# Optimization experiments

Measured on AMD Instinct MI355X. Metric: run time of the kernel, lower is better.

## Reference

```python
import jax, jax.numpy as jnp
import numpy as np

HEADS = 8
DIM_HEAD = 64


def setup_inputs() -> dict:
    key = jax.random.key(0)
    ks = jax.random.split(key, 6)
    B, Nq, Nk, Dq = 4, 2048, 2048, 1024
    inner = HEADS * DIM_HEAD  # 512
    return {
        "x": jax.random.normal(ks[0], (B, Nq, Dq), jnp.float32),
        "context": jax.random.normal(ks[1], (B, Nk, Dq), jnp.float32),
        "Wq": jax.random.normal(ks[2], (Dq, inner), jnp.float32) * 0.02,
        "Wkv": jax.random.normal(ks[3], (Dq, 2 * inner), jnp.float32) * 0.02,
        "Wout": jax.random.normal(ks[4], (inner, Dq), jnp.float32) * 0.02,
        "bout": jax.random.normal(ks[5], (Dq,), jnp.float32) * 0.02,
        "topk": 64,
    }


def reference(x, context, Wq, Wkv, Wout, bout, topk):
    B, Nq, _ = x.shape
    Nk = context.shape[1]
    H, D = HEADS, DIM_HEAD
    scale = D ** -0.5

    # projections: b n (h d) -> b h n d
    q = (x @ Wq).reshape(B, Nq, H, D).transpose(0, 2, 1, 3)
    kv = context @ Wkv
    k, v = jnp.split(kv, 2, axis=-1)
    k = k.reshape(B, Nk, H, D).transpose(0, 2, 1, 3)
    v = v.reshape(B, Nk, H, D).transpose(0, 2, 1, 3)

    sim = jnp.einsum('bhid,bhjd->bhij', q, k) * scale  # [B,H,Nq,Nk]

    # top-k sparsification: keep only topk keys per query, mask rest to -max
    k_eff = min(int(topk), Nk)
    _, idx = jax.lax.top_k(sim, k_eff)  # [B,H,Nq,k_eff]
    keep = jnp.zeros(sim.shape, dtype=bool)
    bi = jnp.arange(B)[:, None, None, None]
    hi = jnp.arange(H)[None, :, None, None]
    qi = jnp.arange(Nq)[None, None, :, None]
    keep = keep.at[bi, hi, qi, idx].set(True)
    max_neg = -jnp.finfo(sim.dtype).max
    sim = jnp.where(keep, sim, max_neg)

    attn = jax.nn.softmax(sim, axis=-1)
    out = jnp.einsum('bhij,bhjd->bhid', attn, v)
    out = out.transpose(0, 2, 1, 3).reshape(B, Nq, H * D)
    return out @ Wout + bout
```

## Files before the change

kernel.cpp:

```cpp
#include <hip/hip_runtime.h>
#include <math.h>

#define BATCH 4
#define NQ 2048
#define NK 2048
#define DQ 1024
#define NHEADS 8
#define DHEAD 64
#define INNER (NHEADS*DHEAD)
#define NROWS (BATCH*NHEADS*NQ)
#define CAND_MAX 128

using frag_ab = __attribute__((ext_vector_type(8))) short;
using frag_cd = __attribute__((ext_vector_type(4))) float;
using u16x8   = __attribute__((ext_vector_type(8))) unsigned short;

static __device__ __forceinline__ unsigned short f32_to_bf16_rne(float f) {
  unsigned u = __float_as_uint(f);
  u += 0x7FFFu + ((u >> 16) & 1u);
  return (unsigned short)(u >> 16);
}

static __device__ __forceinline__ void split_trunc(float f, unsigned short& h, unsigned short& l) {
  unsigned u = __float_as_uint(f);
  h = (unsigned short)(u >> 16);
  float hf = __uint_as_float(u & 0xFFFF0000u);
  unsigned r = __float_as_uint(f - hf);
  l = (unsigned short)(r >> 16);
}

static __device__ __forceinline__ void split3(float f, unsigned short& h,
                                              unsigned short& m, unsigned short& l) {
  unsigned u = __float_as_uint(f);
  h = (unsigned short)(u >> 16);
  float hf = __uint_as_float(u & 0xFFFF0000u);
  float r1 = f - hf;
  unsigned u1 = __float_as_uint(r1);
  m = (unsigned short)(u1 >> 16);
  float mf = __uint_as_float(u1 & 0xFFFF0000u);
  float r2 = r1 - mf;
  l = (unsigned short)(__float_as_uint(r2) >> 16);
}

__global__ __launch_bounds__(256) void split_wT3(
    const float* __restrict__ W, int ldw, int coloff, int K, int N,
    unsigned short* __restrict__ TH, unsigned short* __restrict__ TM,
    unsigned short* __restrict__ TL)
{
  __shared__ float tile[32*33];
  const int k0 = blockIdx.x * 32, n0 = blockIdx.y * 32;
  const int t = threadIdx.x;
  {
    int lk = t >> 3, ln4 = (t & 7) * 4;
    const float4 v = *(const float4*)(W + (size_t)(k0 + lk)*ldw + coloff + n0 + ln4);
    tile[lk*33 + ln4+0] = v.x;
    tile[lk*33 + ln4+1] = v.y;
    tile[lk*33 + ln4+2] = v.z;
    tile[lk*33 + ln4+3] = v.w;
  }
  __syncthreads();
  int n = t >> 3, k4 = (t & 7) * 4;
  #pragma unroll
  for (int j = 0; j < 4; ++j) {
    unsigned short h, m, l;
    split3(tile[(k4+j)*33 + n], h, m, l);
    size_t o = (size_t)(n0 + n)*K + k0 + k4 + j;
    TH[o] = h; TM[o] = m; TL[o] = l;
  }
}

__global__ __launch_bounds__(256) void split_wT(
    const float* __restrict__ W, int ldw, int coloff, int K, int N,
    unsigned short* __restrict__ TH, unsigned short* __restrict__ TL)
{
  __shared__ float tile[32*33];
  const int k0 = blockIdx.x * 32, n0 = blockIdx.y * 32;
  const int t = threadIdx.x;
  {
    int lk = t >> 3, ln4 = (t & 7) * 4;
    const float4 v = *(const float4*)(W + (size_t)(k0 + lk)*ldw + coloff + n0 + ln4);
    tile[lk*33 + ln4+0] = v.x;
    tile[lk*33 + ln4+1] = v.y;
    tile[lk*33 + ln4+2] = v.z;
    tile[lk*33 + ln4+3] = v.w;
  }
  __syncthreads();
  int n = t >> 3, k4 = (t & 7) * 4;
  #pragma unroll
  for (int j = 0; j < 4; ++j) {
    unsigned short h, l;
    split_trunc(tile[(k4+j)*33 + n], h, l);
    TH[(size_t)(n0 + n)*K + k0 + k4 + j] = h;
    TL[(size_t)(n0 + n)*K + k0 + k4 + j] = l;
  }
}

__global__ __launch_bounds__(512) void gemm_mfma6_proj(
    const float* __restrict__ A0,
    const unsigned short* __restrict__ BtH0, const unsigned short* __restrict__ BtM0,
    const unsigned short* __restrict__ BtL0,
    float* __restrict__ C0_, unsigned short* __restrict__ Hi0, unsigned short* __restrict__ Lo0,
    const float* __restrict__ A1,
    const unsigned short* __restrict__ BtH1, const unsigned short* __restrict__ BtM1,
    const unsigned short* __restrict__ BtL1,
    float* __restrict__ C1_, unsigned short* __restrict__ Hi1, unsigned short* __restrict__ Lo1)
{
  extern __shared__ unsigned short smp[];
  unsigned short* ah = smp;
  unsigned short* am = ah + 128*40;
  unsigned short* al = am + 128*40;
  unsigned short* bh = al + 128*40;
  unsigned short* bm = bh + 128*40;
  unsigned short* bl = bm + 128*40;

  const int t = threadIdx.x;
  const int w = t >> 6, l = t & 63;
  const int lr = l & 15, quad = l >> 4;
  const int bid = (int)blockIdx.x;
  const int half = bid >> 8;
  const int b2 = bid & 255;
  const int lid = (b2 & 7) * 32 + (b2 >> 3);
  const int n0 = (lid & 3) * 128, m0 = (lid >> 2) * 128;

  const float* A = half ? A1 : A0;
  const unsigned short* BtH = half ? BtH1 : BtH0;
  const unsigned short* BtM = half ? BtM1 : BtM0;
  const unsigned short* BtL = half ? BtL1 : BtL0;
  float* C32 = half ? C1_ : C0_;
  unsigned short* Hi = half ? Hi1 : Hi0;
  unsigned short* Lo = half ? Lo1 : Lo0;

  frag_cd acc[8];
  #pragma unroll
  for (int nt = 0; nt < 8; ++nt)
    acc[nt] = (frag_cd){0.f, 0.f, 0.f, 0.f};

  for (int kt = 0; kt < DQ; kt += 32) {
    {
      int row = t >> 2, k8 = (t & 3) * 8;
      const float* src = A + (size_t)(m0 + row) * DQ + kt + k8;
      float4 v0 = *(const float4*)(src);
      float4 v1 = *(const float4*)(src + 4);
      float vv[8] = {v0.x, v0.y, v0.z, v0.w, v1.x, v1.y, v1.z, v1.w};
      unsigned short h8[8], m8[8], l8[8];
      #pragma unroll
      for (int j = 0; j < 8; ++j) split3(vv[j], h8[j], m8[j], l8[j]);
      *(u16x8*)(ah + row*40 + k8) = *(u16x8*)h8;
      *(u16x8*)(am + row*40 + k8) = *(u16x8*)m8;
      *(u16x8*)(al + row*40 + k8) = *(u16x8*)l8;
    }
    {
      int n = t >> 2, k8 = (t & 3) * 8;
      size_t o = (size_t)(n0 + n)*DQ + kt + k8;
      *(u16x8*)(bh + n*40 + k8) = *(const u16x8*)(BtH + o);
      *(u16x8*)(bm + n*40 + k8) = *(const u16x8*)(BtM + o);
      *(u16x8*)(bl + n*40 + k8) = *(const u16x8*)(BtL + o);
    }
    __syncthreads();
    {
      int row = w*16 + lr;
      frag_ab aH = *(const frag_ab*)(ah + row*40 + quad*8);
      frag_ab aM = *(const frag_ab*)(am + row*40 + quad*8);
      frag_ab aL = *(const frag_ab*)(al + row*40 + quad*8);
      #pragma unroll
      for (int nt = 0; nt < 8; ++nt) {
        int bn = nt*16 + lr;
        frag_ab bH_ = *(const frag_ab*)(bh + bn*40 + quad*8);
        frag_ab bM_ = *(const frag_ab*)(bm + bn*40 + quad*8);
        frag_ab bL_ = *(const frag_ab*)(bl + bn*40 + quad*8);
        frag_cd c = acc[nt];
        c = __builtin_amdgcn_mfma_f32_16x16x32_bf16(aL, bH_, c, 0, 0, 0);
        c = __builtin_amdgcn_mfma_f32_16x16x32_bf16(aH, bL_, c, 0, 0, 0);
        c = __builtin_amdgcn_mfma_f32_16x16x32_bf16(aM, bM_, c, 0, 0, 0);
        c = __builtin_amdgcn_mfma_f32_16x16x32_bf16(aM, bH_, c, 0, 0, 0);
        c = __builtin_amdgcn_mfma_f32_16x16x32_bf16(aH, bM_, c, 0, 0, 0);
        c = __builtin_amdgcn_mfma_f32_16x16x32_bf16(aH, bH_, c, 0, 0, 0);
        acc[nt] = c;
      }
    }
    __syncthreads();
  }

  #pragma unroll
  for (int nt = 0; nt < 8; ++nt) {
    int cc = n0 + nt*16 + lr;
    int h = cc >> 6, d = cc & 63;
    #pragma unroll
    for (int i = 0; i < 4; ++i) {
      int r = m0 + w*16 + quad*4 + i;
      int b = r >> 11, n = r & (NQ - 1);
      size_t idx = (((size_t)(b*NHEADS + h))*NQ + n)*64 + d;
      float vf = acc[nt][i];
      C32[idx] = vf;
      unsigned short hb = f32_to_bf16_rne(vf);
      float hf = __uint_as_float((unsigned)hb << 16);
      unsigned short lb = f32_to_bf16_rne(vf - hf);
      Hi[idx] = hb;
      Lo[idx] = lb;
    }
  }
}

template<int MODE>
__global__ __launch_bounds__(512) void gemm_mfma3(
    const float* __restrict__ A, int lda,
    const unsigned short* __restrict__ BtH, const unsigned short* __restrict__ BtL,
    int K, int N, const float* __restrict__ bias, float* __restrict__ C0)
{
  __shared__ unsigned short ah[128*40];
  __shared__ unsigned short al[128*40];
  __shared__ unsigned short bh2[128*40];
  __shared__ unsigned short bl2[128*40];
  const int t = threadIdx.x;
  const int w = t >> 6, l = t & 63;
  const int lr = l & 15, quad = l >> 4;
  const int nx = N >> 7;
  const int bid = (int)blockIdx.x;
  const int nwg = (int)gridDim.x;
  const int lid = (bid & 7) * (nwg >> 3) + (bid >> 3);
  const int n0 = (lid % nx) * 128, m0 = (lid / nx) * 128;

  frag_cd acc[8];
  #pragma unroll
  for (int nt = 0; nt < 8; ++nt)
    acc[nt] = (frag_cd){0.f, 0.f, 0.f, 0.f};

  for (int kt = 0; kt < K; kt += 32) {
    {
      int row = t >> 2, k8 = (t & 3) * 8;
      const float* src = A + (size_t)(m0 + row) * lda + kt + k8;
      float4 v0 = *(const float4*)(src);
      float4 v1 = *(const float4*)(src + 4);
      float vv[8] = {v0.x, v0.y, v0.z, v0.w, v1.x, v1.y, v1.z, v1.w};
      unsigned short h8[8], l8[8];
      #pragma unroll
      for (int j = 0; j < 8; ++j) split_trunc(vv[j], h8[j], l8[j]);
      *(u16x8*)(ah + row*40 + k8) = *(u16x8*)h8;
      *(u16x8*)(al + row*40 + k8) = *(u16x8*)l8;
    }
    {
      int n = t >> 2, k8 = (t & 3) * 8;
      size_t o = (size_t)(n0 + n)*K + kt + k8;
      *(u16x8*)(bh2 + n*40 + k8) = *(const u16x8*)(BtH + o);
      *(u16x8*)(bl2 + n*40 + k8) = *(const u16x8*)(BtL + o);
    }
    __syncthreads();
    {
      int row = w*16 + lr;
      frag_ab aH = *(const frag_ab*)(ah + row*40 + quad*8);
      frag_ab aL = *(const frag_ab*)(al + row*40 + quad*8);
      #pragma unroll
      for (int nt = 0; nt < 8; ++nt) {
        int bn = nt*16 + lr;
        frag_ab bH_ = *(const frag_ab*)(bh2 + bn*40 + quad*8);
        frag_ab bL_ = *(const frag_ab*)(bl2 + bn*40 + quad*8);
        acc[nt] = __builtin_amdgcn_mfma_f32_16x16x32_bf16(aH, bH_, acc[nt], 0, 0, 0);
        acc[nt] = __builtin_amdgcn_mfma_f32_16x16x32_bf16(aH, bL_, acc[nt], 0, 0, 0);
        acc[nt] = __builtin_amdgcn_mfma_f32_16x16x32_bf16(aL, bH_, acc[nt], 0, 0, 0);
      }
    }
    __syncthreads();
  }

  #pragma unroll
  for (int nt = 0; nt < 8; ++nt) {
    int cc = n0 + nt*16 + lr;
    #pragma unroll
    for (int i = 0; i < 4; ++i) {
      int r = m0 + w*16 + quad*4 + i;
      float v = acc[nt][i];
      if (MODE == 0) {
        C0[(size_t)r * N + cc] = v + bias[cc];
      } else {
        int b = r >> 11, n = r & (NQ - 1);
        int h = cc >> 6, d = cc & 63;
        C0[(((size_t)(b*NHEADS + h))*NK + n)*64 + d] = v;
      }
    }
  }
}

__global__ __launch_bounds__(512) void score_mfma(
    const unsigned short* __restrict__ Qhi, const unsigned short* __restrict__ Qlo,
    const unsigned short* __restrict__ Khi, const unsigned short* __restrict__ Klo,
    unsigned short* __restrict__ S16, int bh0)
{
  extern __shared__ unsigned short sm[];
  unsigned short* qh = sm;
  unsigned short* ql = qh + 128*72;
  unsigned short* kh = ql + 128*72;
  unsigned short* kl = kh + 128*72;

  const int t  = threadIdx.x;
  const int qt = blockIdx.x, kt = blockIdx.y;
  const int bh = bh0 + blockIdx.z;
  const size_t qbase = ((size_t)bh*NQ + qt*128) * 64;
  const size_t kbase = ((size_t)bh*NK + kt*128) * 64;

  #pragma unroll
  for (int i = 0; i < 2; ++i) {
    int c   = t + i*512;
    int row = c >> 3, off = (c & 7) * 8;
    *(u16x8*)(qh + row*72 + off) = *(const u16x8*)(Qhi + qbase + row*64 + off);
    *(u16x8*)(ql + row*72 + off) = *(const u16x8*)(Qlo + qbase + row*64 + off);
    *(u16x8*)(kh + row*72 + off) = *(const u16x8*)(Khi + kbase + row*64 + off);
    *(u16x8*)(kl + row*72 + off) = *(const u16x8*)(Klo + kbase + row*64 + off);
  }
  __syncthreads();

  const int w = t >> 6, l = t & 63;
  const int quad = l >> 4, lr = l & 15;

  frag_ab aH[2], aL[2];
  {
    int row = w*16 + lr;
    #pragma unroll
    for (int s = 0; s < 2; ++s) {
      aH[s] = *(const frag_ab*)(qh + row*72 + s*32 + quad*8);
      aL[s] = *(const frag_ab*)(ql + row*72 + s*32 + quad*8);
    }
  }

  for (int ks = 0; ks < 8; ++ks) {
    frag_ab bH[2], bL[2];
    int krow = ks*16 + lr;
    #pragma unroll
    for (int s = 0; s < 2; ++s) {
      bH[s] = *(const frag_ab*)(kh + krow*72 + s*32 + quad*8);
      bL[s] = *(const frag_ab*)(kl + krow*72 + s*32 + quad*8);
    }
    frag_cd c = {0.f, 0.f, 0.f, 0.f};
    #pragma unroll
    for (int s = 0; s < 2; ++s) {
      c = __builtin_amdgcn_mfma_f32_16x16x32_bf16(aH[s], bH[s], c, 0, 0, 0);
      c = __builtin_amdgcn_mfma_f32_16x16x32_bf16(aH[s], bL[s], c, 0, 0, 0);
      c = __builtin_amdgcn_mfma_f32_16x16x32_bf16(aL[s], bH[s], c, 0, 0, 0);
    }
    int qrow = qt*128 + w*16 + quad*4;
    int kcol = kt*128 + ks*16 + lr;
    size_t base = ((size_t)blockIdx.z * NQ + qrow) * NK + kcol;
    #pragma unroll
    for (int i = 0; i < 4; ++i) {
      _Float16 h = (_Float16)(c[i] * 0.125f);
      S16[base + (size_t)i*NK] = __builtin_bit_cast(unsigned short, h);
    }
  }
}

__global__ __launch_bounds__(256) void select_rows(
    const unsigned short* __restrict__ S16, unsigned short* __restrict__ cand,
    int* __restrict__ cnt, const int* __restrict__ topkp, int row0)
{
  const int t = threadIdx.x;
  const int w = t >> 6, l = t & 63;
  const int rl = blockIdx.x * 4 + w;
  const size_t row = (size_t)row0 + rl;
  const unsigned short* Sr = S16 + (size_t)rl * NK;
  const unsigned long long lmask = (1ull << l) - 1ull;

  int kEff = *topkp;
  if (kEff > CAND_MAX) kEff = CAND_MAX;
  if (kEff < 1) kEff = 1;

  unsigned uv[32];
  #pragma unroll
  for (int c = 0; c < 32; ++c) {
    unsigned bb = Sr[c*64 + l];
    uv[c] = (bb & 0x8000u) ? (~bb & 0xFFFFu) : (bb | 0x8000u);
  }
  unsigned lo_ = 0u, hi_ = 0xFFFFu;
  while (lo_ < hi_) {
    unsigned mid = (lo_ + hi_ + 1u) >> 1;
    int c_ = 0;
    #pragma unroll
    for (int c = 0; c < 32; ++c) c_ += (uv[c] >= mid) ? 1 : 0;
    #pragma unroll
    for (int off = 32; off > 0; off >>= 1) c_ += __shfl_xor(c_, off);
    if (c_ >= kEff) lo_ = mid; else hi_ = mid - 1;
  }
  unsigned short sb = (lo_ & 0x8000u) ? (unsigned short)(lo_ & 0x7FFFu)
                                      : (unsigned short)(~lo_ & 0xFFFFu);
  float skth = (float)__builtin_bit_cast(_Float16, sb);
  float smarg = skth - 3e-3f;
  _Float16 hm = (_Float16)smarg;
  unsigned short mb = __builtin_bit_cast(unsigned short, hm);
  unsigned um = (mb & 0x8000u) ? (~(unsigned)mb & 0xFFFFu) : ((unsigned)mb | 0x8000u);

  int base = 0;
  for (int c = 0; c < 32; ++c) {
    bool pred = (uv[c] >= um);
    unsigned long long msk = __ballot(pred);
    if (pred) {
      int pos = base + __popcll(msk & lmask);
      if (pos < CAND_MAX) cand[row*CAND_MAX + pos] = (unsigned short)(c*64 + l);
    }
    base += __popcll(msk);
  }
  if (l == 0) cnt[row] = (base < CAND_MAX) ? base : CAND_MAX;
}

__global__ __launch_bounds__(256) void attn_phase_b(
    const float* __restrict__ Q32, const float* __restrict__ K32,
    const float* __restrict__ V32, const unsigned short* __restrict__ cand,
    const int* __restrict__ cnt, float* __restrict__ inner,
    const int* __restrict__ topkp)
{
  __shared__ uint2 pvbuf[4][128];

  const int t = threadIdx.x;
  const int w = t >> 6, l = t & 63;
  const int nwg = (int)gridDim.x;
  const int bid = (int)blockIdx.x;
  const int swz = (bid & 7) * (nwg >> 3) + (bid >> 3);
  const size_t row = (size_t)swz * 4 + w;
  const int bh = (int)(row >> 11);
  const int q  = (int)(row & (NQ - 1));
  const unsigned long long lmask = (1ull << l) - 1ull;

  int kEff = *topkp;
  if (kEff > CAND_MAX) kEff = CAND_MAX;
  if (kEff < 1) kEff = 1;
  int m = cnt[row];
  if (kEff > m) kEff = m;

  const float* Kb = K32 + (size_t)bh * NK * 64;
  const float* Vb = V32 + (size_t)bh * NK * 64;

  const int g4 = l >> 2, r4 = l & 3;
  double q4[4][4];
  #pragma unroll
  for (int i = 0; i < 4; ++i) {
    float4 qf = *(const float4*)(Q32 + row*64 + i*16 + r4*4);
    q4[i][0] = (double)qf.x;
    q4[i][1] = (double)qf.y;
    q4[i][2] = (double)qf.z;
    q4[i][3] = (double)qf.w;
  }

  int ck[2];
  ck[0] = cand[row*CAND_MAX + l];
  ck[1] = cand[row*CAND_MAX + 64 + l];
  double cs[2] = {-INFINITY, -INFINITY};
  unsigned long long cu[2] = {0ull, 0ull};

  #define RESCORE_PASS(P, C)                                                  \
  {                                                                           \
    const int j = (P)*16 + g4;                                                \
    const bool valid = (j < m);                                               \
    int key = __shfl(ck[C], j & 63);                                          \
    const float* kp = Kb + (size_t)(valid ? key : 0) * 64;                    \
    double s0 = 0.0, s1 = 0.0, s2 = 0.0, s3 = 0.0;                            \
    _Pragma("unroll")                                                         \
    for (int i = 0; i < 4; ++i) {                                             \
      float4 kv = *(const float4*)(kp + i*16 + r4*4);                         \
      s0 = fma((double)kv.x, q4[i][0], s0);                                   \
      s1 = fma((double)kv.y, q4[i][1], s1);                                   \
      s2 = fma((double)kv.z, q4[i][2], s2);                                   \
      s3 = fma((double)kv.w, q4[i][3], s3);                                   \
    }                                                                         \
    double s = (s0 + s1) + (s2 + s3);                                         \
    s += __shfl_xor(s, 1);                                                    \
    s += __shfl_xor(s, 2);                                                    \
    s *= 0.125;                                                               \
    double sc = __shfl(s, (l & 15) * 4);                                      \
    const int pp = (P) & 3;                                                   \
    if ((l >> 4) == pp && ((C)*64 + pp*16 + (l & 15)) < m) {                  \
      unsigned long long b = (unsigned long long)__double_as_longlong(sc);    \
      cs[C] = sc;                                                             \
      cu[C] = (b >> 63) ? ~b : (b | 0x8000000000000000ull);                   \
    }                                                                         \
  }

  if (m <= 64) {
    #pragma unroll
    for (int p = 0; p < 4; ++p) RESCORE_PASS(p, 0)
  } else {
    #pragma unroll
    for (int p = 0; p < 4; ++p) RESCORE_PASS(p, 0)
    const int np2 = 4 + ((m - 64 + 15) >> 4);
    for (int p = 4; p < np2; ++p) RESCORE_PASS(p, 1)
  }
  #undef RESCORE_PASS

  const unsigned hu0 = (unsigned)(cu[0] >> 32), lu0 = (unsigned)cu[0];
  const unsigned hu1 = (unsigned)(cu[1] >> 32), lu1 = (unsigned)cu[1];

  unsigned T32 = 0u;
  for (int bit = 31; bit >= 0; --bit) {
    unsigned cT = T32 | (1u << bit);
    int tot = __popcll(__ballot(hu0 >= cT)) + __popcll(__ballot(hu1 >= cT));
    if (tot >= kEff) T32 = cT;
  }
  unsigned Tlo;
  {
    int cgt32 = __popcll(__ballot(hu0 > T32)) + __popcll(__ballot(hu1 > T32));
    bool e0 = (hu0 == T32), e1 = (hu1 == T32);
    unsigned long long bm0 = __ballot(e0), bm1 = __ballot(e1);
    int ceq = __popcll(bm0) + __popcll(bm1);
    int nEq32 = kEff - cgt32;
    if (ceq == 1) {
      Tlo = bm0 ? __shfl(lu0, (int)__builtin_ctzll(bm0))
                : __shfl(lu1, (int)__builtin_ctzll(bm1));
    } else {
      unsigned TL = 0u;
      for (int bit = 31; bit >= 0; --bit) {
        unsigned cT = TL | (1u << bit);
        int tot = __popcll(__ballot(e0 && lu0 >= cT))
                + __popcll(__ballot(e1 && lu1 >= cT));
        if (tot >= nEq32) TL = cT;
      }
      Tlo = TL;
    }
  }
  const unsigned long long T = ((unsigned long long)T32 << 32) | Tlo;

  double s_kth;
  { unsigned long long bb = (T >> 63) ? (T & 0x7FFFFFFFFFFFFFFFull) : ~T;
    s_kth = __longlong_as_double((long long)bb); }

  double nx = -INFINITY;
  #pragma unroll
  for (int c = 0; c < 2; ++c) { double v = (cu[c] < T) ? cs[c] : -INFINITY; nx = fmax(nx, v); }
  #pragma unroll
  for (int off = 32; off > 0; off >>= 1) nx = fmax(nx, __shfl_xor(nx, off));

  double smax = fmax(cs[0], cs[1]);
  #pragma unroll
  for (int off = 32; off > 0; off >>= 1) smax = fmax(smax, __shfl_xor(smax, off));

  const double DELTA = 5e-6;
  float wgt[2];
  if (!(s_kth - nx < 2.0*DELTA)) {
    int cgt = __popcll(__ballot(cu[0] > T)) + __popcll(__ballot(cu[1] > T));
    int nEq = kEff - cgt;
    int eqBase = 0;
    #pragma unroll
    for (int c = 0; c < 2; ++c) {
      bool eq = (cu[c] == T);
      unsigned long long eqm = __ballot(eq);
      int er = __popcll(eqm & lmask);
      bool sel = (cu[c] > T) || (eq && (eqBase + er) < nEq);
      eqBase += __popcll(eqm);
      wgt[c] = sel ? expf((float)(cs[c] - smax)) : 0.f;
    }
  } else {
    double cmid = 0.5 * (s_kth + nx);
    #pragma unroll
    for (int c = 0; c < 2; ++c) {
      double mu = 0.5 + (cs[c] - cmid) / (2.0*DELTA);
      mu = fmin(1.0, fmax(0.0, mu));
      wgt[c] = (float)mu * expf((float)(cs[c] - smax));
    }
  }

  pvbuf[w][l]      = make_uint2((unsigned)ck[0] & (NK - 1), __float_as_uint(wgt[0]));
  pvbuf[w][64 + l] = make_uint2((unsigned)ck[1] & (NK - 1), __float_as_uint(wgt[1]));
  float wsum = wgt[0] + wgt[1];
  #pragma unroll
  for (int off = 32; off > 0; off >>= 1) wsum += __shfl_xor(wsum, off);
  asm volatile("s_waitcnt lgkmcnt(0)" ::: "memory");

  const int sub = l >> 4;
  const int dl  = l & 15;
  const float* Vb4 = Vb + dl * 4;
  float ax = 0.f, ay = 0.f, az = 0.f, aw = 0.f;
  const int mm4 = (m + 3) & ~3;
  #pragma unroll 4
  for (int j0 = 0; j0 < mm4; j0 += 4) {
    uint2 p = pvbuf[w][j0 + sub];
    float wj = __uint_as_float(p.y);
    const float4 v = *(const float4*)(Vb4 + ((size_t)p.x << 6));
    ax = fmaf(wj, v.x, ax);
    ay = fmaf(wj, v.y, ay);
    az = fmaf(wj, v.z, az);
    aw = fmaf(wj, v.w, aw);
  }
  #pragma unroll
  for (int off = 32; off >= 16; off >>= 1) {
    ax += __shfl_xor(ax, off);
    ay += __shfl_xor(ay, off);
    az += __shfl_xor(az, off);
    aw += __shfl_xor(aw, off);
  }
  if (sub == 0) {
    int b = bh >> 3, h = bh & 7;
    float inv = 1.0f / wsum;
    float4 o;
    o.x = ax * inv; o.y = ay * inv; o.z = az * inv; o.w = aw * inv;
    *(float4*)(inner + ((size_t)b*NQ + q)*INNER + h*DHEAD + dl*4) = o;
  }
}

extern "C" void kernel_launch(void* const* d_in, const int* in_sizes, int n_in,
                              void* d_out, int out_size, void* d_ws, size_t ws_size,
                              hipStream_t stream)
{
  const float* x    = (const float*)d_in[0];
  const float* ctx  = (const float*)d_in[1];
  const float* Wq   = (const float*)d_in[2];
  const float* Wkv  = (const float*)d_in[3];
  const float* Wout = (const float*)d_in[4];
  const float* bout = (const float*)d_in[5];
  const int*   topk = (const int*)d_in[6];
  float* out = (float*)d_out;

  const size_t SZ = (size_t)BATCH * NHEADS * NQ * DHEAD;

  size_t off = 0;
  char* base = (char*)d_ws;
  auto take = [&](size_t bytes) { char* r = base + off; off += (bytes + 255) & ~(size_t)255; return r; };
  float* Q32 = (float*)take(SZ * sizeof(float));
  float* K32 = (float*)take(SZ * sizeof(float));
  unsigned short* cand = (unsigned short*)take((size_t)NROWS * CAND_MAX * 2);
  int* cnt = (int*)take((size_t)NROWS * sizeof(int));
  unsigned short* Qhi = (unsigned short*)take(SZ * 2);
  unsigned short* Qlo = (unsigned short*)take(SZ * 2);
  unsigned short* Khi = (unsigned short*)take(SZ * 2);
  unsigned short* Klo = (unsigned short*)take(SZ * 2);
  char* slab = base + off;

  const size_t WSZ = (size_t)INNER * DQ * 2;
  unsigned short* WqTH = (unsigned short*)(slab + 0*WSZ);
  unsigned short* WqTM = (unsigned short*)(slab + 1*WSZ);
  unsigned short* WqTL = (unsigned short*)(slab + 2*WSZ);
  unsigned short* WkTH = (unsigned short*)(slab + 3*WSZ);
  unsigned short* WkTM = (unsigned short*)(slab + 4*WSZ);
  unsigned short* WkTL = (unsigned short*)(slab + 5*WSZ);
  unsigned short* S16 = (unsigned short*)slab;
  unsigned short* WvTH = (unsigned short*)(slab + 0*WSZ);
  unsigned short* WvTL = (unsigned short*)(slab + 1*WSZ);
  unsigned short* WoTH = (unsigned short*)(slab + 2*WSZ);
  unsigned short* WoTL = (unsigned short*)(slab + 3*WSZ);
  float* V32   = (float*)Qhi;
  float* inner = (float*)Khi;

  const size_t per_bh = (size_t)NQ * NK * sizeof(unsigned short);
  size_t avail = (ws_size > off) ? (ws_size - off) : 0;
  int bhchunk = (int)(avail / per_bh);
  if (bhchunk < 1)  bhchunk = 1;
  if (bhchunk > 32) bhchunk = 32;

  const int M = BATCH * NQ;
  const int SCORE_LDS = 4 * 128 * 72 * (int)sizeof(unsigned short);
  const int PROJ_LDS  = 6 * 128 * 40 * (int)sizeof(unsigned short);
  hipFuncSetAttribute(reinterpret_cast<const void*>(score_mfma),
                      hipFuncAttributeMaxDynamicSharedMemorySize, SCORE_LDS);
  hipFuncSetAttribute(reinterpret_cast<const void*>(gemm_mfma6_proj),
                      hipFuncAttributeMaxDynamicSharedMemorySize, PROJ_LDS);

  split_wT3<<<dim3(DQ/32, INNER/32), 256, 0, stream>>>(Wq,  INNER,   0, DQ, INNER, WqTH, WqTM, WqTL);
  split_wT3<<<dim3(DQ/32, INNER/32), 256, 0, stream>>>(Wkv, 2*INNER, 0, DQ, INNER, WkTH, WkTM, WkTL);

  gemm_mfma6_proj<<<dim3(512), 512, PROJ_LDS, stream>>>(
      x,   WqTH, WqTM, WqTL, Q32, Qhi, Qlo,
      ctx, WkTH, WkTM, WkTL, K32, Khi, Klo);

  for (int c0 = 0; c0 < BATCH*NHEADS; c0 += bhchunk) {
    int cc = BATCH*NHEADS - c0; if (cc > bhchunk) cc = bhchunk;
    score_mfma<<<dim3(NQ/128, NK/128, cc), 512, SCORE_LDS, stream>>>(
        Qhi, Qlo, Khi, Klo, S16, c0);
    select_rows<<<dim3(cc*NQ/4), 256, 0, stream>>>(S16, cand, cnt, topk, c0*NQ);
  }

  split_wT<<<dim3(DQ/32, INNER/32), 256, 0, stream>>>(Wkv, 2*INNER, INNER, DQ, INNER, WvTH, WvTL);
  split_wT<<<dim3(INNER/32, DQ/32), 256, 0, stream>>>(Wout, DQ, 0, INNER, DQ, WoTH, WoTL);

  gemm_mfma3<2><<<dim3((INNER/128)*(M/128)), 512, 0, stream>>>(ctx, DQ, WvTH, WvTL, DQ, INNER, nullptr, V32);
  attn_phase_b<<<dim3(NROWS/4), 256, 0, stream>>>(Q32, K32, V32, cand, cnt, inner, topk);
  gemm_mfma3<0><<<dim3((DQ/128)*(M/128)), 512, 0, stream>>>(inner, INNER, WoTH, WoTL, INNER, DQ, bout, out);
}
```

Before: 700.8 us.

## Vectorize S16 score stores via permuted key layout and rebalance rescore lanes

The score kernel now holds all eight 16x16 accumulator tiles and writes each row as one 16-byte vector store, instead of scattered 2-byte stores. This permutes the column order inside each 128-key tile, so select_rows un-permutes candidate indices back to true key ids. Separately, the fp64 rescore pass in attn_phase_b now uses 8 lanes per candidate with float2 loads instead of 4 lanes with float4 loads. That doubles the number of passes but shortens each lane's dependent FMA chain, and the extra shuffle step and higher register pressure from c8 are the cost.

After: 706.2 us. Within noise of the previous version (+0.8%).

```diff
diff --git a/kernel.cpp b/kernel.cpp
--- a/kernel.cpp
+++ b/kernel.cpp
@@ -321,6 +321,8 @@
     }
   }
 
+  frag_cd c8[8];
+  #pragma unroll
   for (int ks = 0; ks < 8; ++ks) {
     frag_ab bH[2], bL[2];
     int krow = ks*16 + lr;
@@ -336,14 +338,20 @@
       c = __builtin_amdgcn_mfma_f32_16x16x32_bf16(aH[s], bL[s], c, 0, 0, 0);
       c = __builtin_amdgcn_mfma_f32_16x16x32_bf16(aL[s], bH[s], c, 0, 0, 0);
     }
-    int qrow = qt*128 + w*16 + quad*4;
-    int kcol = kt*128 + ks*16 + lr;
-    size_t base = ((size_t)blockIdx.z * NQ + qrow) * NK + kcol;
-    #pragma unroll
-    for (int i = 0; i < 4; ++i) {
-      _Float16 h = (_Float16)(c[i] * 0.125f);
-      S16[base + (size_t)i*NK] = __builtin_bit_cast(unsigned short, h);
-    }
+    c8[ks] = c;
+  }
+
+  #pragma unroll
+  for (int i = 0; i < 4; ++i) {
+    unsigned short o8[8];
+    #pragma unroll
+    for (int ks = 0; ks < 8; ++ks) {
+      _Float16 h = (_Float16)(c8[ks][i] * 0.125f);
+      o8[ks] = __builtin_bit_cast(unsigned short, h);
+    }
+    int qrow = qt*128 + w*16 + quad*4 + i;
+    size_t base = ((size_t)blockIdx.z * NQ + qrow) * NK + kt*128 + lr*8;
+    *(u16x8*)(S16 + base) = *(u16x8*)o8;
   }
 }
 
@@ -392,7 +400,11 @@
     unsigned long long msk = __ballot(pred);
     if (pred) {
       int pos = base + __popcll(msk & lmask);
-      if (pos < CAND_MAX) cand[row*CAND_MAX + pos] = (unsigned short)(c*64 + l);
+      if (pos < CAND_MAX) {
+        unsigned p = (unsigned)c * 64u + (unsigned)l;
+        unsigned key = (p & 0xFF80u) | ((p & 7u) << 4) | ((p >> 3) & 15u);
+        cand[row*CAND_MAX + pos] = (unsigned short)key;
+      }
     }
     base += __popcll(msk);
   }
@@ -426,15 +438,13 @@
   const float* Kb = K32 + (size_t)bh * NK * 64;
   const float* Vb = V32 + (size_t)bh * NK * 64;
 
-  const int g4 = l >> 2, r4 = l & 3;
-  double q4[4][4];
+  const int g = l >> 3, r = l & 7;
+  double2 q2[4];
   #pragma unroll
   for (int i = 0; i < 4; ++i) {
-    float4 qf = *(const float4*)(Q32 + row*64 + i*16 + r4*4);
-    q4[i][0] = (double)qf.x;
-    q4[i][1] = (double)qf.y;
-    q4[i][2] = (double)qf.z;
-    q4[i][3] = (double)qf.w;
+    float2 qf = *(const float2*)(Q32 + row*64 + i*16 + r*2);
+    q2[i].x = (double)qf.x;
+    q2[i].y = (double)qf.y;
   }
 
   int ck[2];
@@ -445,26 +455,25 @@
 
   #define RESCORE_PASS(P, C)                                                  \
   {                                                                           \
-    const int j = (P)*16 + g4;                                                \
+    const int j = (P)*8 + g;                                                  \
     const bool valid = (j < m);                                               \
     int key = __shfl(ck[C], j & 63);                                          \
     const float* kp = Kb + (size_t)(valid ? key : 0) * 64;                    \
-    double s0 = 0.0, s1 = 0.0, s2 = 0.0, s3 = 0.0;                            \
+    double s0 = 0.0, s1 = 0.0;                                                \
     _Pragma("unroll")                                                         \
     for (int i = 0; i < 4; ++i) {                                             \
-      float4 kv = *(const float4*)(kp + i*16 + r4*4);                         \
-      s0 = fma((double)kv.x, q4[i][0], s0);                                   \
-      s1 = fma((double)kv.y, q4[i][1], s1);                                   \
-      s2 = fma((double)kv.z, q4[i][2], s2);                                   \
-      s3 = fma((double)kv.w, q4[i][3], s3);                                   \
+      float2 kv = *(const float2*)(kp + i*16 + r*2);                          \
+      s0 = fma((double)kv.x, q2[i].x, s0);                                    \
+      s1 = fma((double)kv.y, q2[i].y, s1);                                    \
     }                                                                         \
-    double s = (s0 + s1) + (s2 + s3);                                         \
+    double s = s0 + s1;                                                       \
     s += __shfl_xor(s, 1);                                                    \
     s += __shfl_xor(s, 2);                                                    \
+    s += __shfl_xor(s, 4);                                                    \
     s *= 0.125;                                                               \
-    double sc = __shfl(s, (l & 15) * 4);                                      \
-    const int pp = (P) & 3;                                                   \
-    if ((l >> 4) == pp && ((C)*64 + pp*16 + (l & 15)) < m) {                  \
+    double sc = __shfl(s, (l & 7) * 8);                                       \
+    const int pp = (P) & 7;                                                   \
+    if ((l >> 3) == pp && ((C)*64 + pp*8 + (l & 7)) < m) {                    \
       unsigned long long b = (unsigned long long)__double_as_longlong(sc);    \
       cs[C] = sc;                                                             \
       cu[C] = (b >> 63) ? ~b : (b | 0x8000000000000000ull);                   \
@@ -473,12 +482,12 @@
 
   if (m <= 64) {
     #pragma unroll
-    for (int p = 0; p < 4; ++p) RESCORE_PASS(p, 0)
+    for (int p = 0; p < 8; ++p) RESCORE_PASS(p, 0)
   } else {
     #pragma unroll
-    for (int p = 0; p < 4; ++p) RESCORE_PASS(p, 0)
-    const int np2 = 4 + ((m - 64 + 15) >> 4);
-    for (int p = 4; p < np2; ++p) RESCORE_PASS(p, 1)
+    for (int p = 0; p < 8; ++p) RESCORE_PASS(p, 0)
+    const int np2 = 8 + ((m - 64 + 7) >> 3);
+    for (int p = 8; p < np2; ++p) RESCORE_PASS(p, 1)
   }
   #undef RESCORE_PASS
 
```
